# Optimization experiments

Hardware: AMD Instinct MI355X
Metric: run time of the kernel (lower is better)

## Reference

```python
import jax, jax.numpy as jnp
import numpy as np

V, E, L, T, H, B = 8124, 1024, 24, 512, 16, 2
S = E // H
DFF = E * 8 // 3  # 2730
EPS = 1e-5
SCALE = 1.0 / np.sqrt(E)  # note: 1/sqrt(emb_dim), as in the source


def _pe():
    # sinusoidal positional encoding [T, E]
    pos = jnp.arange(T, dtype=jnp.float32)[:, None]
    div = jnp.exp(jnp.arange(0, E, 2, dtype=jnp.float32) * (-np.log(10000.0) / E))
    pe = jnp.zeros((T, E), jnp.float32)
    pe = pe.at[:, 0::2].set(jnp.sin(pos * div))
    pe = pe.at[:, 1::2].set(jnp.cos(pos * div))
    return pe


def _rms(x, g):
    # NOTE: source takes the mean over the WHOLE tensor (no dim arg)
    rms = jnp.sqrt(jnp.mean(x.astype(jnp.float32) ** 2) + EPS)
    return (x / rms * g).astype(x.dtype)


def setup_inputs() -> dict:
    key = jax.random.key(0)
    ks = jax.random.split(key, 9)
    def w(k, shape):
        return jax.random.normal(k, shape, jnp.float32) * 0.02
    return {
        "tokens": jax.random.randint(ks[0], (B, T), 0, V),
        "emb_table": w(ks[1], (V, E)),
        "Wqkv": w(ks[2], (L, E, 3 * E)), "bqkv": jnp.zeros((L, 3 * E), jnp.float32),
        "Wo": w(ks[3], (L, E, E)), "bo": jnp.zeros((L, E), jnp.float32),
        "W1": w(ks[4], (L, E, DFF)), "b1": jnp.zeros((L, DFF), jnp.float32),
        "W3": w(ks[5], (L, E, DFF)), "b3": jnp.zeros((L, DFF), jnp.float32),
        "W2": w(ks[6], (L, DFF, E)), "b2": jnp.zeros((L, E), jnp.float32),
        "g_mha": jnp.ones((L, E), jnp.float32),
        "g_ff": jnp.ones((L, E), jnp.float32),
        "g_final": jnp.ones((E,), jnp.float32),
        "Wout": w(ks[7], (E, V)), "bout": jnp.zeros((V,), jnp.float32),
    }


def reference(tokens, emb_table, Wqkv, bqkv, Wo, bo, W1, b1, W3, b3, W2, b2,
              g_mha, g_ff, g_final, Wout, bout):
    x = emb_table[tokens] + _pe()[None]  # [B,T,E]
    mask = jnp.tril(jnp.ones((T, T), bool))

    def block(x, p):
        wqkv, bq, wo, bo_, w1, b1_, w3, b3_, w2, b2_, gm, gf = p
        # --- causal MHA ---
        y = _rms(x, gm)
        qkv = (y @ wqkv + bq).reshape(B, T, H, 3, S)
        q = qkv[..., 0, :].transpose(0, 2, 1, 3)  # [B,H,T,S]
        k = qkv[..., 1, :].transpose(0, 2, 1, 3)
        v = qkv[..., 2, :].transpose(0, 2, 1, 3)
        attn = jnp.einsum('bhqd,bhkd->bhqk', q, k).astype(jnp.float32) * SCALE
        attn = jnp.where(mask, attn, -jnp.inf)
        attn = jax.nn.softmax(attn, axis=-1).astype(x.dtype)
        y = jnp.einsum('bhqk,bhkd->bhqd', attn, v)
        y = y.transpose(0, 2, 1, 3).reshape(B, T, E)
        x = x + (y @ wo + bo_)
        # --- SwiGLU FFN ---
        h = _rms(x, gf)
        u = h @ w1 + b1_
        u = u * jax.nn.sigmoid(u) * (h @ w3 + b3_)
        return x + (u @ w2 + b2_), None

    x, _ = jax.lax.scan(block, x, (Wqkv, bqkv, Wo, bo, W1, b1, W3, b3, W2, b2, g_mha, g_ff))
    return _rms(x, g_final) @ Wout + bout  # [B,T,V]
```

## Files before the change

kernel.cpp:

```cpp
#include <hip/hip_runtime.h>
#include <hip/hip_bf16.h>
#include <math.h>

#define EDIM   1024
#define TSEQ   512
#define NBATCH 2
#define NHEAD  16
#define HDIM   64
#define NLAYER 24
#define VOCAB  8124
#define DFFDIM 2730
#define DPAD   2752
#define MTOK   (NBATCH*TSEQ)
#define NELEM  (MTOK*EDIM)
#define EPSF   1e-5f
#define SCALEF (1.0f/32.0f)
#define NEGBIG (-1e30f)

typedef __bf16 bf16x8 __attribute__((ext_vector_type(8)));
typedef __bf16 bf16x4 __attribute__((ext_vector_type(4)));
typedef float  f32x4  __attribute__((ext_vector_type(4)));

#define MFMA(a, b, c) __builtin_amdgcn_mfma_f32_16x16x32_bf16((a), (b), (c), 0, 0, 0)

__device__ __forceinline__ void gl_lds16(const __bf16* g, __bf16* l) {
  __builtin_amdgcn_global_load_lds(
      (const __attribute__((address_space(1))) void*)g,
      (__attribute__((address_space(3))) void*)l, 16, 0, 0);
}

__global__ __launch_bounds__(256) void k_embed(const int* __restrict__ tok,
                                               const float* __restrict__ emb,
                                               float* __restrict__ x) {
  const int bt = blockIdx.x;
  const int t  = bt & (TSEQ - 1);
  const int tk = tok[bt];
  const float* er = emb + (size_t)tk * EDIM;
  float* xr = x + (size_t)bt * EDIM;
  for (int e = threadIdx.x * 4; e < EDIM; e += 256 * 4) {
    float4 v = *(const float4*)(er + e);
    float vv[4] = {v.x, v.y, v.z, v.w};
    float ou[4];
#pragma unroll
    for (int j = 0; j < 4; ++j) {
      int ee = e + j;
      int i2 = ee & ~1;
      float freq = expf(-(float)i2 * (9.210340371976184f / 1024.0f));
      float ang  = (float)t * freq;
      ou[j] = vv[j] + ((ee & 1) ? cosf(ang) : sinf(ang));
    }
    *(float4*)(xr + e) = make_float4(ou[0], ou[1], ou[2], ou[3]);
  }
}

__global__ __launch_bounds__(256) void k_red1f(float* __restrict__ x,
                                               const float* __restrict__ p0,
                                               const float* __restrict__ p1,
                                               const float* __restrict__ bias,
                                               float* __restrict__ part) {
  float s = 0.f;
  const bool fold = (p0 != nullptr);
  for (int i = (blockIdx.x * 256 + threadIdx.x) * 4; i < NELEM; i += 256 * 256 * 4) {
    float4 v = *(const float4*)(x + i);
    if (fold) {
      float4 a = *(const float4*)(p0 + i);
      float4 b = *(const float4*)(p1 + i);
      float4 c = *(const float4*)(bias + (i & (EDIM - 1)));
      v.x += a.x + b.x + c.x; v.y += a.y + b.y + c.y;
      v.z += a.z + b.z + c.z; v.w += a.w + b.w + c.w;
      *(float4*)(x + i) = v;
    }
    s += v.x * v.x + v.y * v.y + v.z * v.z + v.w * v.w;
  }
#pragma unroll
  for (int o = 32; o > 0; o >>= 1) s += __shfl_down(s, o);
  __shared__ float sm[4];
  if ((threadIdx.x & 63) == 0) sm[threadIdx.x >> 6] = s;
  __syncthreads();
  if (threadIdx.x == 0) part[blockIdx.x] = sm[0] + sm[1] + sm[2] + sm[3];
}

__global__ __launch_bounds__(256) void k_red2(const float* __restrict__ part,
                                              float* __restrict__ scale) {
  float s = part[threadIdx.x];
#pragma unroll
  for (int o = 32; o > 0; o >>= 1) s += __shfl_down(s, o);
  __shared__ float sm[4];
  if ((threadIdx.x & 63) == 0) sm[threadIdx.x >> 6] = s;
  __syncthreads();
  if (threadIdx.x == 0) {
    float tot = sm[0] + sm[1] + sm[2] + sm[3];
    scale[0] = 1.0f / sqrtf(tot / (float)NELEM + EPSF);
  }
}

__global__ __launch_bounds__(256) void k_rms_bf(const float* __restrict__ x,
                                                const float* __restrict__ g,
                                                const float* __restrict__ scal,
                                                __bf16* __restrict__ y) {
  const float sc = scal[0];
  const int i = (blockIdx.x * 256 + threadIdx.x) * 4;
  float4 v  = *(const float4*)(x + i);
  float4 gv = *(const float4*)(g + (i & (EDIM - 1)));
  bf16x4 o = {(__bf16)(v.x * sc * gv.x), (__bf16)(v.y * sc * gv.y),
              (__bf16)(v.z * sc * gv.z), (__bf16)(v.w * sc * gv.w)};
  *(bf16x4*)(y + i) = o;
}

__device__ __forceinline__ void conv_tile(const float* __restrict__ src,
                                          __bf16* __restrict__ dst,
                                          int K, int N, int Kpad, int tk, int tn) {
  __shared__ float st[64][65];
  const int k0 = tk << 6, n0 = tn << 6;
  const int tid = threadIdx.x;
  const int r0 = tid >> 4, c4 = (tid & 15) << 2;
#pragma unroll
  for (int i = 0; i < 4; ++i) {
    const int r = r0 + i * 16;
    const int k = k0 + r;
    float4 v = make_float4(0.f, 0.f, 0.f, 0.f);
    if (k < K) {
      const float* sp = src + (size_t)k * N + n0 + c4;
      if (n0 + c4 + 3 < N) v = *(const float4*)sp;
      else {
        if (n0 + c4 + 0 < N) v.x = sp[0];
        if (n0 + c4 + 1 < N) v.y = sp[1];
        if (n0 + c4 + 2 < N) v.z = sp[2];
        if (n0 + c4 + 3 < N) v.w = sp[3];
      }
    }
    st[r][c4 + 0] = v.x; st[r][c4 + 1] = v.y; st[r][c4 + 2] = v.z; st[r][c4 + 3] = v.w;
  }
  __syncthreads();
#pragma unroll
  for (int i = 0; i < 4; ++i) {
    const int rr = r0 + i * 16;
    bf16x4 o = {(__bf16)st[c4 + 0][rr], (__bf16)st[c4 + 1][rr],
                (__bf16)st[c4 + 2][rr], (__bf16)st[c4 + 3][rr]};
    *(bf16x4*)&dst[(size_t)(n0 + rr) * Kpad + k0 + c4] = o;
  }
}

__global__ __launch_bounds__(256) void k_convL(const float* __restrict__ Wqkv,
                                               const float* __restrict__ Wo,
                                               const float* __restrict__ W1,
                                               const float* __restrict__ W3,
                                               const float* __restrict__ W2w,
                                               __bf16* qkvT, __bf16* woT,
                                               __bf16* w1T, __bf16* w3T, __bf16* w2T) {
  const int b = blockIdx.x;
  if (b < 768)       { conv_tile(Wqkv, qkvT, 1024, 3072, 1024, b / 48, b % 48); }
  else if (b < 1024) { int t = b - 768;  conv_tile(Wo,  woT,  1024, 1024, 1024, t / 16, t % 16); }
  else if (b < 1712) { int t = b - 1024; conv_tile(W1,  w1T,  1024, 2730, 1024, t / 43, t % 43); }
  else if (b < 2400) { int t = b - 1712; conv_tile(W3,  w3T,  1024, 2730, 1024, t / 43, t % 43); }
  else               { int t = b - 2400; conv_tile(W2w, w2T,  2730, 1024, 2752, t / 16, t % 16); }
}

__global__ __launch_bounds__(256) void k_convH(const float* __restrict__ Wout,
                                               __bf16* __restrict__ WoutT) {
  conv_tile(Wout, WoutT, 1024, VOCAB, 1024, blockIdx.x / 127, blockIdx.x % 127);
}

template <int BM, int MODE>
__global__ __launch_bounds__(256) void mm(
    const __bf16* __restrict__ A, const __bf16* __restrict__ B0w,
    const __bf16* __restrict__ B1w,
    const float* __restrict__ bias0, const float* __restrict__ bias1,
    float* __restrict__ po, __bf16* __restrict__ ob,
    __bf16* __restrict__ qout, __bf16* __restrict__ kout, __bf16* __restrict__ vout,
    int N, int lda, int ldb, int Ktot) {
  constexpr int DUAL = (MODE == 2) ? 2 : 1;
  constexpr int FM = BM / 64;
  constexpr int NA = BM / 32;
  __shared__ __bf16 As[2][8][BM][8];
  __shared__ __bf16 Bs[2][DUAL][8][64][8];
  const int tid = threadIdx.x, lane = tid & 63, wave = tid >> 6;
  const int m0 = blockIdx.y * BM, n0 = blockIdx.x << 6;
  const int wrow0 = wave * (BM / 4);
  const int lr = lane & 15, kh = lane >> 4;

  const int ktiles = Ktot >> 6;
  const int nt0 = (ktiles + gridDim.z - 1) / gridDim.z;
  const int tbeg = blockIdx.z * nt0;
  const int tend = (ktiles < tbeg + nt0) ? ktiles : (tbeg + nt0);
  const int nt = tend - tbeg;

  f32x4 acc[DUAL][FM][4];
#pragma unroll
  for (int d = 0; d < DUAL; ++d)
#pragma unroll
    for (int mi = 0; mi < FM; ++mi)
#pragma unroll
      for (int ni = 0; ni < 4; ++ni) acc[d][mi][ni] = (f32x4){0.f, 0.f, 0.f, 0.f};

  auto STAGE = [&](int buf, int t) {
    const int k0 = (tbeg + t) << 6;
#pragma unroll
    for (int i = 0; i < NA; ++i) {
      const int d = i * 256 + tid;
      const int kb2 = d / BM, row = d % BM;
      gl_lds16(A + (size_t)(m0 + row) * lda + k0 + kb2 * 8, &As[buf][kb2][row][0]);
    }
#pragma unroll
    for (int i = 0; i < 2; ++i) {
      const int d = i * 256 + tid;
      const int kb2 = d >> 6, col = d & 63;
      gl_lds16(B0w + (size_t)(n0 + col) * ldb + k0 + kb2 * 8, &Bs[buf][0][kb2][col][0]);
      if (MODE == 2)
        gl_lds16(B1w + (size_t)(n0 + col) * ldb + k0 + kb2 * 8, &Bs[buf][DUAL - 1][kb2][col][0]);
    }
  };
  auto COMP = [&](int buf) {
#pragma unroll
    for (int ks = 0; ks < 2; ++ks) {
      const int kidx = ks * 4 + kh;
      bf16x8 af[FM];
#pragma unroll
      for (int mi = 0; mi < FM; ++mi)
        af[mi] = *(const bf16x8*)&As[buf][kidx][wrow0 + mi * 16 + lr][0];
#pragma unroll
      for (int d = 0; d < DUAL; ++d)
#pragma unroll
        for (int ni = 0; ni < 4; ++ni) {
          bf16x8 bfr = *(const bf16x8*)&Bs[buf][d][kidx][ni * 16 + lr][0];
#pragma unroll
          for (int mi = 0; mi < FM; ++mi)
            acc[d][mi][ni] = MFMA(af[mi], bfr, acc[d][mi][ni]);
        }
    }
  };

  STAGE(0, 0);
  __syncthreads();
  for (int t = 0; t + 1 < nt; ++t) {
    STAGE((t + 1) & 1, t + 1);
    COMP(t & 1);
    __syncthreads();
  }
  COMP((nt - 1) & 1);

#pragma unroll
  for (int mi = 0; mi < FM; ++mi)
#pragma unroll
    for (int ni = 0; ni < 4; ++ni) {
      const int col = n0 + ni * 16 + lr;
      if (MODE == 0) {
        const float bs = bias0[col];
        const int h = col / (3 * HDIM);
        const int rsel = (col >> 6) % 3;
        const int s2 = col & (HDIM - 1);
#pragma unroll
        for (int j = 0; j < 4; ++j) {
          const int row = m0 + wrow0 + mi * 16 + (kh << 2) + j;
          const int b = row >> 9, t = row & (TSEQ - 1);
          const float v = acc[0][mi][ni][j] + bs;
          if (rsel == 0)      qout[((size_t)(b * NHEAD + h) * TSEQ + t) * HDIM + s2] = (__bf16)v;
          else if (rsel == 1) kout[((size_t)(b * NHEAD + h) * TSEQ + t) * HDIM + s2] = (__bf16)v;
          else                vout[((size_t)(b * NHEAD + h) * HDIM + s2) * TSEQ + t] = (__bf16)v;
        }
      } else if (MODE == 1) {
        float* pz = po + (size_t)blockIdx.z * MTOK * EDIM;
#pragma unroll
        for (int j = 0; j < 4; ++j) {
          const int row = m0 + wrow0 + mi * 16 + (kh << 2) + j;
          pz[(size_t)row * EDIM + col] = acc[0][mi][ni][j];
        }
      } else if (MODE == 2) {
        const bool ok = col < N;
        const float bb1 = ok ? bias0[col] : 0.f;
        const float bb3 = ok ? bias1[col] : 0.f;
#pragma unroll
        for (int j = 0; j < 4; ++j) {
          const int row = m0 + wrow0 + mi * 16 + (kh << 2) + j;
          const float a1v = acc[0][mi][ni][j] + bb1;
          const float a3v = acc[DUAL - 1][mi][ni][j] + bb3;
          const float v = a1v * (1.0f / (1.0f + __expf(-a1v))) * a3v;
          ob[(size_t)row * DPAD + col] = (__bf16)v;
        }
      } else {
        if (col < N) {
          const float bs = bias0[col];
#pragma unroll
          for (int j = 0; j < 4; ++j) {
            const int row = m0 + wrow0 + mi * 16 + (kh << 2) + j;
            po[(size_t)row * N + col] = acc[0][mi][ni][j] + bs;
          }
        }
      }
    }
}

__global__ __launch_bounds__(256) void k_flash(const __bf16* __restrict__ qbuf,
                                               const __bf16* __restrict__ kbuf,
                                               const __bf16* __restrict__ vbufT,
                                               __bf16* __restrict__ y2) {
  const int qt = blockIdx.x, bh = blockIdx.y;
  const int b = bh >> 4, h = bh & 15;
  const int m0 = qt << 6;
  const __bf16* qp = qbuf  + (size_t)bh * TSEQ * HDIM;
  const __bf16* kp = kbuf  + (size_t)bh * TSEQ * HDIM;
  const __bf16* vp = vbufT + (size_t)bh * HDIM * TSEQ;
  __shared__ __bf16 Qs[8][64][8], Ks[8][64][8], Vs[8][64][8], Ps[8][64][8];
  __shared__ float wmax[2][64], wsum[2][64];
  const int tid = threadIdx.x, lane = tid & 63, wave = tid >> 6;
  const int wm = (wave >> 1) << 5, wn = (wave & 1) << 5;
  const int lr = lane & 15, kh = lane >> 4;

#pragma unroll
  for (int i = 0; i < 2; ++i) {
    const int d = i * 256 + tid;
    const int kb2 = d >> 6, row = d & 63;
    gl_lds16(qp + (size_t)(m0 + row) * HDIM + kb2 * 8, &Qs[kb2][row][0]);
  }
  float m_[2][4], l_[2][4];
#pragma unroll
  for (int mi = 0; mi < 2; ++mi)
#pragma unroll
    for (int j = 0; j < 4; ++j) { m_[mi][j] = NEGBIG; l_[mi][j] = 0.f; }
  f32x4 o00 = {0,0,0,0}, o01 = {0,0,0,0}, o10 = {0,0,0,0}, o11 = {0,0,0,0};

  for (int kt = 0; kt <= qt; ++kt) {
    const int n0 = kt << 6;
    __syncthreads();
#pragma unroll
    for (int i = 0; i < 2; ++i) {
      const int d = i * 256 + tid;
      const int kb2 = d >> 6, row = d & 63;
      gl_lds16(kp + (size_t)(n0 + row) * HDIM + kb2 * 8, &Ks[kb2][row][0]);
      gl_lds16(vp + (size_t)row * TSEQ + n0 + kb2 * 8, &Vs[kb2][row][0]);
    }
    __syncthreads();

    f32x4 s00 = {0,0,0,0}, s01 = {0,0,0,0}, s10 = {0,0,0,0}, s11 = {0,0,0,0};
#pragma unroll
    for (int ks = 0; ks < 2; ++ks) {
      const int kidx = ks * 4 + kh;
      bf16x8 a0 = *(const bf16x8*)&Qs[kidx][wm + lr][0];
      bf16x8 a1 = *(const bf16x8*)&Qs[kidx][wm + 16 + lr][0];
      bf16x8 b0 = *(const bf16x8*)&Ks[kidx][wn + lr][0];
      bf16x8 b1 = *(const bf16x8*)&Ks[kidx][wn + 16 + lr][0];
      s00 = MFMA(a0, b0, s00); s01 = MFMA(a0, b1, s01);
      s10 = MFMA(a1, b0, s10); s11 = MFMA(a1, b1, s11);
    }
    float pv_[2][2][4];
#pragma unroll
    for (int mi = 0; mi < 2; ++mi)
#pragma unroll
      for (int j = 0; j < 4; ++j) {
        const int grow = m0 + wm + mi * 16 + (kh << 2) + j;
        float best = NEGBIG;
#pragma unroll
        for (int ni = 0; ni < 2; ++ni) {
          f32x4 sfr = (mi == 0) ? (ni == 0 ? s00 : s01) : (ni == 0 ? s10 : s11);
          const int gcol = n0 + wn + ni * 16 + lr;
          float t = sfr[j] * SCALEF;
          if (gcol > grow) t = NEGBIG;
          pv_[mi][ni][j] = t;
          best = fmaxf(best, t);
        }
        float v = best;
        v = fmaxf(v, __shfl_xor(v, 1)); v = fmaxf(v, __shfl_xor(v, 2));
        v = fmaxf(v, __shfl_xor(v, 4)); v = fmaxf(v, __shfl_xor(v, 8));
        wmax[wave & 1][wm + mi * 16 + (kh << 2) + j] = v;
      }
    __syncthreads();

    float alpha[2][4];
#pragma unroll
    for (int mi = 0; mi < 2; ++mi)
#pragma unroll
      for (int j = 0; j < 4; ++j) {
        const int rl = wm + mi * 16 + (kh << 2) + j;
        const float tmax = fmaxf(wmax[0][rl], wmax[1][rl]);
        const float mn = fmaxf(m_[mi][j], tmax);
        alpha[mi][j] = __expf(m_[mi][j] - mn);
        m_[mi][j] = mn;
        float rs = 0.f;
#pragma unroll
        for (int ni = 0; ni < 2; ++ni) {
          const float p = __expf(pv_[mi][ni][j] - mn);
          pv_[mi][ni][j] = p;
          rs += p;
        }
        rs += __shfl_xor(rs, 1); rs += __shfl_xor(rs, 2);
        rs += __shfl_xor(rs, 4); rs += __shfl_xor(rs, 8);
        wsum[wave & 1][rl] = rs;
      }
#pragma unroll
    for (int mi = 0; mi < 2; ++mi)
#pragma unroll
      for (int ni = 0; ni < 2; ++ni)
#pragma unroll
        for (int j = 0; j < 4; ++j) {
          const int prow = wm + mi * 16 + (kh << 2) + j;
          const int pcol = wn + ni * 16 + lr;
          Ps[pcol >> 3][prow][pcol & 7] = (__bf16)pv_[mi][ni][j];
        }
    __syncthreads();

#pragma unroll
    for (int mi = 0; mi < 2; ++mi)
#pragma unroll
      for (int j = 0; j < 4; ++j) {
        const int rl = wm + mi * 16 + (kh << 2) + j;
        l_[mi][j] = l_[mi][j] * alpha[mi][j] + wsum[0][rl] + wsum[1][rl];
      }
#pragma unroll
    for (int j = 0; j < 4; ++j) {
      o00[j] *= alpha[0][j]; o01[j] *= alpha[0][j];
      o10[j] *= alpha[1][j]; o11[j] *= alpha[1][j];
    }
#pragma unroll
    for (int ks = 0; ks < 2; ++ks) {
      const int kidx = ks * 4 + kh;
      bf16x8 a0 = *(const bf16x8*)&Ps[kidx][wm + lr][0];
      bf16x8 a1 = *(const bf16x8*)&Ps[kidx][wm + 16 + lr][0];
      bf16x8 b0 = *(const bf16x8*)&Vs[kidx][wn + lr][0];
      bf16x8 b1 = *(const bf16x8*)&Vs[kidx][wn + 16 + lr][0];
      o00 = MFMA(a0, b0, o00); o01 = MFMA(a0, b1, o01);
      o10 = MFMA(a1, b0, o10); o11 = MFMA(a1, b1, o11);
    }
  }

#pragma unroll
  for (int mi = 0; mi < 2; ++mi)
#pragma unroll
    for (int ni = 0; ni < 2; ++ni) {
      f32x4 oo = (mi == 0) ? (ni == 0 ? o00 : o01) : (ni == 0 ? o10 : o11);
      const int col = wn + ni * 16 + lr;
#pragma unroll
      for (int j = 0; j < 4; ++j) {
        const int row = m0 + wm + mi * 16 + (kh << 2) + j;
        y2[((size_t)(b * TSEQ) + row) * EDIM + h * HDIM + col] = (__bf16)(oo[j] / l_[mi][j]);
      }
    }
}

extern "C" void kernel_launch(void* const* d_in, const int* in_sizes, int n_in,
                              void* d_out, int out_size, void* d_ws, size_t ws_size,
                              hipStream_t stream) {
  const int*   tokens  = (const int*)d_in[0];
  const float* emb     = (const float*)d_in[1];
  const float* Wqkv    = (const float*)d_in[2];
  const float* bqkv    = (const float*)d_in[3];
  const float* Wo      = (const float*)d_in[4];
  const float* bo      = (const float*)d_in[5];
  const float* W1      = (const float*)d_in[6];
  const float* b1      = (const float*)d_in[7];
  const float* W3      = (const float*)d_in[8];
  const float* b3      = (const float*)d_in[9];
  const float* W2w     = (const float*)d_in[10];
  const float* b2      = (const float*)d_in[11];
  const float* g_mha   = (const float*)d_in[12];
  const float* g_ff    = (const float*)d_in[13];
  const float* g_final = (const float*)d_in[14];
  const float* Wout    = (const float*)d_in[15];
  const float* bout    = (const float*)d_in[16];
  float* out = (float*)d_out;

  char* base = (char*)d_ws;
  size_t off = 0;
  auto alloc = [&](size_t bytes) { char* p = base + off; off = (off + bytes + 255) & ~(size_t)255; return p; };
  float*  x    = (float*)alloc(4u << 20);
  float*  part = (float*)alloc(2048);
  float*  scal = (float*)alloc(256);
  __bf16* ybf  = (__bf16*)alloc(2u << 20);
  __bf16* qbf  = (__bf16*)alloc(2u << 20);
  __bf16* kbf  = (__bf16*)alloc(2u << 20);
  __bf16* vbT  = (__bf16*)alloc(2u << 20);
  __bf16* y2bf = (__bf16*)alloc(2u << 20);
  __bf16* ubf  = (__bf16*)alloc((size_t)MTOK * DPAD * 2);
  float*  pbuf = (float*)alloc((size_t)2 * MTOK * EDIM * 4);
  __bf16* qkvT = (__bf16*)alloc((size_t)3072 * 1024 * 2);
  __bf16* woT  = (__bf16*)alloc((size_t)1024 * 1024 * 2);
  __bf16* w1T  = (__bf16*)alloc((size_t)2752 * 1024 * 2);
  __bf16* w3T  = (__bf16*)alloc((size_t)2752 * 1024 * 2);
  __bf16* w2T  = (__bf16*)alloc((size_t)1024 * 2752 * 2);
  __bf16* WoutT = qkvT;

  k_embed<<<MTOK, 256, 0, stream>>>(tokens, emb, x);

  const float* pend_bias = nullptr;
  for (int l = 0; l < NLAYER; ++l) {
    k_convL<<<3088, 256, 0, stream>>>(
        Wqkv + (size_t)l * EDIM * 3 * EDIM, Wo + (size_t)l * EDIM * EDIM,
        W1 + (size_t)l * EDIM * DFFDIM, W3 + (size_t)l * EDIM * DFFDIM,
        W2w + (size_t)l * DFFDIM * EDIM, qkvT, woT, w1T, w3T, w2T);
    k_red1f<<<256, 256, 0, stream>>>(x, pend_bias ? pbuf : nullptr,
                                     pbuf + (size_t)MTOK * EDIM, pend_bias, part);
    k_red2<<<1, 256, 0, stream>>>(part, scal);
    k_rms_bf<<<1024, 256, 0, stream>>>(x, g_mha + (size_t)l * EDIM, scal, ybf);
    mm<128, 0><<<dim3(48, 8, 1), 256, 0, stream>>>(
        ybf, qkvT, nullptr, bqkv + (size_t)l * 3 * EDIM, nullptr,
        nullptr, nullptr, qbf, kbf, vbT, 3072, 1024, 1024, 1024);
    k_flash<<<dim3(8, 32), 256, 0, stream>>>(qbf, kbf, vbT, y2bf);
    mm<64, 1><<<dim3(16, 16, 2), 256, 0, stream>>>(
        y2bf, woT, nullptr, nullptr, nullptr,
        pbuf, nullptr, nullptr, nullptr, nullptr, 1024, 1024, 1024, 1024);
    k_red1f<<<256, 256, 0, stream>>>(x, pbuf, pbuf + (size_t)MTOK * EDIM,
                                     bo + (size_t)l * EDIM, part);
    k_red2<<<1, 256, 0, stream>>>(part, scal);
    k_rms_bf<<<1024, 256, 0, stream>>>(x, g_ff + (size_t)l * EDIM, scal, ybf);
    mm<128, 2><<<dim3(43, 8, 1), 256, 0, stream>>>(
        ybf, w1T, w3T, b1 + (size_t)l * DFFDIM, b3 + (size_t)l * DFFDIM,
        nullptr, ubf, nullptr, nullptr, nullptr, DFFDIM, 1024, 1024, 1024);
    mm<64, 1><<<dim3(16, 16, 2), 256, 0, stream>>>(
        ubf, w2T, nullptr, nullptr, nullptr,
        pbuf, nullptr, nullptr, nullptr, nullptr, 1024, DPAD, 2752, 2752);
    pend_bias = b2 + (size_t)l * EDIM;
  }

  k_red1f<<<256, 256, 0, stream>>>(x, pbuf, pbuf + (size_t)MTOK * EDIM, pend_bias, part);
  k_red2<<<1, 256, 0, stream>>>(part, scal);
  k_rms_bf<<<1024, 256, 0, stream>>>(x, g_final, scal, ybf);
  k_convH<<<2032, 256, 0, stream>>>(Wout, WoutT);
  mm<128, 3><<<dim3(127, 8, 1), 256, 0, stream>>>(
      ybf, WoutT, nullptr, bout, nullptr,
      out, nullptr, nullptr, nullptr, nullptr, VOCAB, 1024, 1024, 1024);
}
```

Before: 4.307 ms.

## Double-buffer flash KV loads, use vmcnt waits in GEMM, fuse RMS scale kernels

The flash-attention kernel now double-buffers its K/V tiles, prefetching the next tile while computing the current one. Several full __syncthreads are replaced by explicit s_waitcnt plus s_barrier, so waves wait only on the loads they need. The GEMM main loop uses vmcnt-based waits instead of full syncs, letting the next stage's loads stay in flight during compute. The single-block scale reduction is folded into the RMS normalize kernel, removing two launches per layer, though every block now redoes the small 256-entry reduction.

```diff
diff --git a/kernel.cpp b/kernel.cpp
--- a/kernel.cpp
+++ b/kernel.cpp
@@ -27,6 +27,14 @@
   __builtin_amdgcn_global_load_lds(
       (const __attribute__((address_space(1))) void*)g,
       (__attribute__((address_space(3))) void*)l, 16, 0, 0);
+}
+
+template <int N> __device__ __forceinline__ void vmwait() {
+  asm volatile("s_waitcnt vmcnt(%0)" :: "n"(N) : "memory");
+}
+__device__ __forceinline__ void lgkm_barrier() {
+  asm volatile("s_waitcnt lgkmcnt(0)" ::: "memory");
+  __builtin_amdgcn_s_barrier();
 }
 
 __global__ __launch_bounds__(256) void k_embed(const int* __restrict__ tok,
@@ -80,31 +88,23 @@
   if (threadIdx.x == 0) part[blockIdx.x] = sm[0] + sm[1] + sm[2] + sm[3];
 }
 
-__global__ __launch_bounds__(256) void k_red2(const float* __restrict__ part,
-                                              float* __restrict__ scale) {
+__global__ __launch_bounds__(256) void k_rms2(const float* __restrict__ x,
+                                              const float* __restrict__ g,
+                                              const float* __restrict__ part,
+                                              __bf16* __restrict__ y) {
   float s = part[threadIdx.x];
 #pragma unroll
   for (int o = 32; o > 0; o >>= 1) s += __shfl_down(s, o);
   __shared__ float sm[4];
   if ((threadIdx.x & 63) == 0) sm[threadIdx.x >> 6] = s;
   __syncthreads();
-  if (threadIdx.x == 0) {
-    float tot = sm[0] + sm[1] + sm[2] + sm[3];
-    scale[0] = 1.0f / sqrtf(tot / (float)NELEM + EPSF);
-  }
-}
-
-__global__ __launch_bounds__(256) void k_rms_bf(const float* __restrict__ x,
-                                                const float* __restrict__ g,
-                                                const float* __restrict__ scal,
-                                                __bf16* __restrict__ y) {
-  const float sc = scal[0];
+  const float sc = 1.0f / sqrtf((sm[0] + sm[1] + sm[2] + sm[3]) / (float)NELEM + EPSF);
   const int i = (blockIdx.x * 256 + threadIdx.x) * 4;
   float4 v  = *(const float4*)(x + i);
   float4 gv = *(const float4*)(g + (i & (EDIM - 1)));
-  bf16x4 o = {(__bf16)(v.x * sc * gv.x), (__bf16)(v.y * sc * gv.y),
-              (__bf16)(v.z * sc * gv.z), (__bf16)(v.w * sc * gv.w)};
-  *(bf16x4*)(y + i) = o;
+  bf16x4 o4 = {(__bf16)(v.x * sc * gv.x), (__bf16)(v.y * sc * gv.y),
+               (__bf16)(v.z * sc * gv.z), (__bf16)(v.w * sc * gv.w)};
+  *(bf16x4*)(y + i) = o4;
 }
 
 __device__ __forceinline__ void conv_tile(const float* __restrict__ src,
@@ -172,6 +172,7 @@
   constexpr int DUAL = (MODE == 2) ? 2 : 1;
   constexpr int FM = BM / 64;
   constexpr int NA = BM / 32;
+  constexpr int LOADS = NA + 2 * DUAL;
   __shared__ __bf16 As[2][8][BM][8];
   __shared__ __bf16 Bs[2][DUAL][8][64][8];
   const int tid = threadIdx.x, lane = tid & 63, wave = tid >> 6;
@@ -231,13 +232,18 @@
   };
 
   STAGE(0, 0);
-  __syncthreads();
-  for (int t = 0; t + 1 < nt; ++t) {
-    STAGE((t + 1) & 1, t + 1);
-    COMP(t & 1);
-    __syncthreads();
-  }
-  COMP((nt - 1) & 1);
+  int cur = 0;
+  for (int t = 0; t < nt - 1; ++t) {
+    STAGE(cur ^ 1, t + 1);
+    vmwait<LOADS>();
+    __builtin_amdgcn_s_barrier();
+    COMP(cur);
+    __builtin_amdgcn_s_barrier();
+    cur ^= 1;
+  }
+  vmwait<0>();
+  __builtin_amdgcn_s_barrier();
+  COMP(cur);
 
 #pragma unroll
   for (int mi = 0; mi < FM; ++mi)
@@ -300,18 +306,31 @@
   const __bf16* qp = qbuf  + (size_t)bh * TSEQ * HDIM;
   const __bf16* kp = kbuf  + (size_t)bh * TSEQ * HDIM;
   const __bf16* vp = vbufT + (size_t)bh * HDIM * TSEQ;
-  __shared__ __bf16 Qs[8][64][8], Ks[8][64][8], Vs[8][64][8], Ps[8][64][8];
+  __shared__ __bf16 Qs[8][64][8], Ks[2][8][64][8], Vs[2][8][64][8], Ps[8][64][8];
   __shared__ float wmax[2][64], wsum[2][64];
   const int tid = threadIdx.x, lane = tid & 63, wave = tid >> 6;
   const int wm = (wave >> 1) << 5, wn = (wave & 1) << 5;
   const int lr = lane & 15, kh = lane >> 4;
 
+  auto STAGE_KV = [&](int kt2, int buf) {
+    const int n0s = kt2 << 6;
+#pragma unroll
+    for (int i = 0; i < 2; ++i) {
+      const int d = i * 256 + tid;
+      const int kb2 = d >> 6, row = d & 63;
+      gl_lds16(kp + (size_t)(n0s + row) * HDIM + kb2 * 8, &Ks[buf][kb2][row][0]);
+      gl_lds16(vp + (size_t)row * TSEQ + n0s + kb2 * 8, &Vs[buf][kb2][row][0]);
+    }
+  };
+
 #pragma unroll
   for (int i = 0; i < 2; ++i) {
     const int d = i * 256 + tid;
     const int kb2 = d >> 6, row = d & 63;
     gl_lds16(qp + (size_t)(m0 + row) * HDIM + kb2 * 8, &Qs[kb2][row][0]);
   }
+  STAGE_KV(0, 0);
+
   float m_[2][4], l_[2][4];
 #pragma unroll
   for (int mi = 0; mi < 2; ++mi)
@@ -319,17 +338,16 @@
     for (int j = 0; j < 4; ++j) { m_[mi][j] = NEGBIG; l_[mi][j] = 0.f; }
   f32x4 o00 = {0,0,0,0}, o01 = {0,0,0,0}, o10 = {0,0,0,0}, o11 = {0,0,0,0};
 
+  int cur = 0;
   for (int kt = 0; kt <= qt; ++kt) {
     const int n0 = kt << 6;
-    __syncthreads();
-#pragma unroll
-    for (int i = 0; i < 2; ++i) {
-      const int d = i * 256 + tid;
-      const int kb2 = d >> 6, row = d & 63;
-      gl_lds16(kp + (size_t)(n0 + row) * HDIM + kb2 * 8, &Ks[kb2][row][0]);
-      gl_lds16(vp + (size_t)row * TSEQ + n0 + kb2 * 8, &Vs[kb2][row][0]);
-    }
-    __syncthreads();
+    if (kt < qt) {
+      STAGE_KV(kt + 1, cur ^ 1);
+      vmwait<4>();
+    } else {
+      vmwait<0>();
+    }
+    __builtin_amdgcn_s_barrier();
 
     f32x4 s00 = {0,0,0,0}, s01 = {0,0,0,0}, s10 = {0,0,0,0}, s11 = {0,0,0,0};
 #pragma unroll
@@ -337,8 +355,8 @@
       const int kidx = ks * 4 + kh;
       bf16x8 a0 = *(const bf16x8*)&Qs[kidx][wm + lr][0];
       bf16x8 a1 = *(const bf16x8*)&Qs[kidx][wm + 16 + lr][0];
-      bf16x8 b0 = *(const bf16x8*)&Ks[kidx][wn + lr][0];
-      bf16x8 b1 = *(const bf16x8*)&Ks[kidx][wn + 16 + lr][0];
+      bf16x8 b0 = *(const bf16x8*)&Ks[cur][kidx][wn + lr][0];
+      bf16x8 b1 = *(const bf16x8*)&Ks[cur][kidx][wn + 16 + lr][0];
       s00 = MFMA(a0, b0, s00); s01 = MFMA(a0, b1, s01);
       s10 = MFMA(a1, b0, s10); s11 = MFMA(a1, b1, s11);
     }
@@ -363,7 +381,7 @@
         v = fmaxf(v, __shfl_xor(v, 4)); v = fmaxf(v, __shfl_xor(v, 8));
         wmax[wave & 1][wm + mi * 16 + (kh << 2) + j] = v;
       }
-    __syncthreads();
+    lgkm_barrier();
 
     float alpha[2][4];
 #pragma unroll
@@ -396,7 +414,7 @@
           const int pcol = wn + ni * 16 + lr;
           Ps[pcol >> 3][prow][pcol & 7] = (__bf16)pv_[mi][ni][j];
         }
-    __syncthreads();
+    lgkm_barrier();
 
 #pragma unroll
     for (int mi = 0; mi < 2; ++mi)
@@ -415,11 +433,13 @@
       const int kidx = ks * 4 + kh;
       bf16x8 a0 = *(const bf16x8*)&Ps[kidx][wm + lr][0];
       bf16x8 a1 = *(const bf16x8*)&Ps[kidx][wm + 16 + lr][0];
-      bf16x8 b0 = *(const bf16x8*)&Vs[kidx][wn + lr][0];
-      bf16x8 b1 = *(const bf16x8*)&Vs[kidx][wn + 16 + lr][0];
+      bf16x8 b0 = *(const bf16x8*)&Vs[cur][kidx][wn + lr][0];
+      bf16x8 b1 = *(const bf16x8*)&Vs[cur][kidx][wn + 16 + lr][0];
       o00 = MFMA(a0, b0, o00); o01 = MFMA(a0, b1, o01);
       o10 = MFMA(a1, b0, o10); o11 = MFMA(a1, b1, o11);
     }
+    __builtin_amdgcn_s_barrier();
+    cur ^= 1;
   }
 
 #pragma unroll
@@ -463,7 +483,6 @@
   auto alloc = [&](size_t bytes) { char* p = base + off; off = (off + bytes + 255) & ~(size_t)255; return p; };
   float*  x    = (float*)alloc(4u << 20);
   float*  part = (float*)alloc(2048);
-  float*  scal = (float*)alloc(256);
   __bf16* ybf  = (__bf16*)alloc(2u << 20);
   __bf16* qbf  = (__bf16*)alloc(2u << 20);
   __bf16* kbf  = (__bf16*)alloc(2u << 20);
@@ -488,8 +507,7 @@
         W2w + (size_t)l * DFFDIM * EDIM, qkvT, woT, w1T, w3T, w2T);
     k_red1f<<<256, 256, 0, stream>>>(x, pend_bias ? pbuf : nullptr,
                                      pbuf + (size_t)MTOK * EDIM, pend_bias, part);
-    k_red2<<<1, 256, 0, stream>>>(part, scal);
-    k_rms_bf<<<1024, 256, 0, stream>>>(x, g_mha + (size_t)l * EDIM, scal, ybf);
+    k_rms2<<<1024, 256, 0, stream>>>(x, g_mha + (size_t)l * EDIM, part, ybf);
     mm<128, 0><<<dim3(48, 8, 1), 256, 0, stream>>>(
         ybf, qkvT, nullptr, bqkv + (size_t)l * 3 * EDIM, nullptr,
         nullptr, nullptr, qbf, kbf, vbT, 3072, 1024, 1024, 1024);
@@ -499,8 +517,7 @@
         pbuf, nullptr, nullptr, nullptr, nullptr, 1024, 1024, 1024, 1024);
     k_red1f<<<256, 256, 0, stream>>>(x, pbuf, pbuf + (size_t)MTOK * EDIM,
                                      bo + (size_t)l * EDIM, part);
-    k_red2<<<1, 256, 0, stream>>>(part, scal);
-    k_rms_bf<<<1024, 256, 0, stream>>>(x, g_ff + (size_t)l * EDIM, scal, ybf);
+    k_rms2<<<1024, 256, 0, stream>>>(x, g_ff + (size_t)l * EDIM, part, ybf);
     mm<128, 2><<<dim3(43, 8, 1), 256, 0, stream>>>(
         ybf, w1T, w3T, b1 + (size_t)l * DFFDIM, b3 + (size_t)l * DFFDIM,
         nullptr, ubf, nullptr, nullptr, nullptr, DFFDIM, 1024, 1024, 1024);
@@ -511,8 +528,7 @@
   }
 
   k_red1f<<<256, 256, 0, stream>>>(x, pbuf, pbuf + (size_t)MTOK * EDIM, pend_bias, part);
-  k_red2<<<1, 256, 0, stream>>>(part, scal);
-  k_rms_bf<<<1024, 256, 0, stream>>>(x, g_final, scal, ybf);
+  k_rms2<<<1024, 256, 0, stream>>>(x, g_final, part, ybf);
   k_convH<<<2032, 256, 0, stream>>>(Wout, WoutT);
   mm<128, 3><<<dim3(127, 8, 1), 256, 0, stream>>>(
       ybf, WoutT, nullptr, bout, nullptr,
```

Result: faster. 4.021 ms (-6.6%).
